# Performance work log

Hardware: AMD Instinct MI355X
Metric: run time of the kernel (lower is better)

## Reference

```python
import jax, jax.numpy as jnp
import numpy as np

B, H, L, D = 2, 16, 1024, 64
LMAX = 2048  # max_sequence_length: patterns built & normalized at LMAX, then sliced to L
PI = float(np.pi)


def _scale_pattern(freq):
    # pattern[h, t, d] = exp(i(t+ph)) + exp(i(2t+ph)) + exp(i(0.5t+ph)), ph = 2*pi*h/H
    # identical across d, so keep [H, L, 1] and broadcast over D
    phase = 2.0 * PI * jnp.arange(H, dtype=jnp.float32) / H          # [H]
    t = jnp.linspace(0.0, 2.0 * PI * freq, LMAX)                     # [LMAX]
    a1 = t[None, :] + phase[:, None]
    a2 = 2.0 * t[None, :] + phase[:, None]
    a3 = 0.5 * t[None, :] + phase[:, None]
    pr = jnp.cos(a1) + jnp.cos(a2) + jnp.cos(a3)                     # [H, LMAX]
    pi_ = jnp.sin(a1) + jnp.sin(a2) + jnp.sin(a3)
    norm = jnp.sqrt(jnp.sum(pr * pr + pi_ * pi_, axis=1, keepdims=True))  # over full LMAX
    pr, pi_ = pr / norm, pi_ / norm
    return pr[:, :L, None], pi_[:, :L, None]                          # [H, L, 1]


def _expert_total_pattern():
    # 8 experts x 3 aspects; pattern[t, d] = exp(i(f*t + 2*pi*d/D)), normalized per
    # column over LMAX (|exp|=1 -> norm sqrt(LMAX)). Elementwise complex multiply is
    # linear, so the expert stage equals x * sum(all patterns)/(sqrt(3)*sqrt(8)).
    freqs = np.array([[0.3 + 0.1 * i, 0.2 + 0.1 * i, 0.1 + 0.1 * i]
                      for i in range(8)], dtype=np.float32).reshape(-1)   # [24]
    t = jnp.linspace(0.0, 2.0 * PI, LMAX)                                 # [LMAX]
    phase_d = 2.0 * PI * jnp.arange(D, dtype=jnp.float32) / D             # [D]
    ang = jnp.asarray(freqs)[:, None, None] * t[None, :, None] + phase_d[None, None, :]  # [24, LMAX, D]
    col_norm = 1.0 / np.sqrt(float(LMAX))
    denom = np.sqrt(3.0) * np.sqrt(8.0)
    pr = jnp.sum(jnp.cos(ang), axis=0) * (col_norm / denom)               # [LMAX, D]
    pi_ = jnp.sum(jnp.sin(ang), axis=0) * (col_norm / denom)
    return pr[:L], pi_[:L]                                                # [L, D]


def _process_scale(Qr, Qi, Kr, Ki, Vr, Vi, pr, pi_):
    # complex elementwise pattern multiply
    Qpr = Qr * pr - Qi * pi_
    Qpi = Qr * pi_ + Qi * pr
    Kpr = Kr * pr - Ki * pi_
    Kpi = Kr * pi_ + Ki * pr
    # complex scores = Qp @ Kp^T (no conjugation, matching the torch code)
    sr = jnp.einsum('bhld,bhmd->bhlm', Qpr, Kpr) - jnp.einsum('bhld,bhmd->bhlm', Qpi, Kpi)
    si = jnp.einsum('bhld,bhmd->bhlm', Qpr, Kpi) + jnp.einsum('bhld,bhmd->bhlm', Qpi, Kpr)
    mag = jnp.sqrt(sr * sr + si * si) / np.sqrt(float(D))
    w = jax.nn.softmax(mag, axis=-1)
    return (jnp.einsum('bhlm,bhmd->bhld', w, Vr),
            jnp.einsum('bhlm,bhmd->bhld', w, Vi))


def reference(Q_real, Q_imag, K_real, K_imag, V_real, V_imag):
    scale_freqs = [1.0, 0.5, 0.25, 0.1]  # char, word, phrase, sentence
    acc_r = jnp.zeros_like(Q_real)
    acc_i = jnp.zeros_like(Q_real)
    for f in scale_freqs:
        pr, pi_ = _scale_pattern(f)
        o_r, o_i = _process_scale(Q_real, Q_imag, K_real, K_imag, V_real, V_imag, pr, pi_)
        acc_r = acc_r + o_r
        acc_i = acc_i + o_i
    inv = 1.0 / np.sqrt(float(len(scale_freqs)))
    acc_r = acc_r * inv
    acc_i = acc_i * inv
    # expert mixing (linear in x -> single fused complex elementwise multiply)
    epr, epi = _expert_total_pattern()  # [L, D], broadcast over B,H
    out_r = acc_r * epr - acc_i * epi
    out_i = acc_r * epi + acc_i * epr
    return jnp.stack([out_r, out_i], axis=0)  # [2, B, H, L, D] (real, imag)


def setup_inputs() -> dict:
    key = jax.random.key(0)
    ks = jax.random.split(key, 6)
    shape = (B, H, L, D)
    names = ['Q_real', 'Q_imag', 'K_real', 'K_imag', 'V_real', 'V_imag']
    return {n: jax.random.normal(k, shape, dtype=jnp.float32) for n, k in zip(names, ks)}
```

## Files before the change

### kernel.cpp

```cpp
#include <hip/hip_runtime.h>
#include <math.h>

typedef short bf16x8 __attribute__((ext_vector_type(8)));
typedef float f32x4 __attribute__((ext_vector_type(4)));

#define BDIM 256
constexpr int B_ = 2, H_ = 16, L_ = 1024, D_ = 64, LMAX_ = 2048;
constexpr int BH_ = B_ * H_;
constexpr float PI_F = 3.14159265358979323846f;

constexpr int WS_SVP = 0;
constexpr int WS_KBR = 65536;
constexpr int WS_KBI = WS_KBR + 1048576;
constexpr int WS_VTR = WS_KBI + 1048576;
constexpr int WS_VTI = WS_VTR + 1048576;

__device__ __forceinline__ unsigned short f2b(float x) {
    union { float f; unsigned u; } v; v.f = x;
    return (unsigned short)((v.u + 0x8000u) >> 16);
}
__device__ __forceinline__ float b2f(unsigned short x) {
    union { unsigned u; float f; } v; v.u = ((unsigned)x) << 16;
    return v.f;
}
__device__ __forceinline__ unsigned pk2(float a, float b) {
    union { float f; unsigned u; } va, vb; va.f = a; vb.f = b;
    return ((va.u + 0x8000u) >> 16) | ((vb.u + 0x8000u) & 0xFFFF0000u);
}
__device__ __forceinline__ uint4 pack4(const float4& a, const float4& b) {
    return make_uint4(pk2(a.x, a.y), pk2(a.z, a.w), pk2(b.x, b.y), pk2(b.z, b.w));
}
__device__ __forceinline__ unsigned cvtpk(float lo, float hi) {
    unsigned r;
    asm("v_cvt_pk_bf16_f32 %0, %1, %2" : "=v"(r) : "v"(lo), "v"(hi));
    return r;
}
__device__ __forceinline__ float vsqrt(float x) {
    float r;
    asm("v_sqrt_f32 %0, %1" : "=v"(r) : "v"(x));
    return r;
}

#define MFMA(a, b, c) __builtin_amdgcn_mfma_f32_16x16x32_bf16((a), (b), (c), 0, 0, 0)

__device__ __forceinline__ float a_val(int s, int l, float4 invn) {
    const float fr = (s == 0) ? 1.0f : (s == 1) ? 0.5f : (s == 2) ? 0.25f : 0.1f;
    const float iv = (s == 0) ? invn.x : (s == 1) ? invn.y : (s == 2) ? invn.z : invn.w;
    float t = (2.0f * PI_F * fr / (float)(LMAX_ - 1)) * (float)l;
    float m2 = 3.0f + 2.0f * cosf(t) + 2.0f * cosf(0.5f * t) + 2.0f * cosf(1.5f * t);
    return sqrtf(fmaxf(m2, 0.0f)) * iv;
}

__global__ __launch_bounds__(BDIM)
void prep_kernel(const float* __restrict__ Kr, const float* __restrict__ Ki,
                 const float* __restrict__ Vr, const float* __restrict__ Vi,
                 float* __restrict__ ws) {
    const int tid = threadIdx.x;
    const int blk = blockIdx.x;
    unsigned short* KbR = (unsigned short*)(ws + WS_KBR);
    unsigned short* KbI = (unsigned short*)(ws + WS_KBI);
    unsigned short* VtR = (unsigned short*)(ws + WS_VTR);
    unsigned short* VtI = (unsigned short*)(ws + WS_VTI);

    if (blk < 256) {
        const int comp = blk >> 7;
        const float* src = comp ? Ki : Kr;
        unsigned short* dst = comp ? KbI : KbR;
        size_t b0 = (size_t)(blk & 127) * 16384;
#pragma unroll
        for (int i = 0; i < 4; ++i) {
            size_t e = b0 + (size_t)(i * 256 + tid) * 16;
            float4 x0 = *(const float4*)(src + e);
            float4 x1 = *(const float4*)(src + e + 4);
            float4 x2 = *(const float4*)(src + e + 8);
            float4 x3 = *(const float4*)(src + e + 12);
            *(uint4*)(dst + e) = pack4(x0, x1);
            *(uint4*)(dst + e + 8) = pack4(x2, x3);
        }
    } else {
        __shared__ unsigned short sT[64 * 70];
        __shared__ float sRed[4 * 64];
        const int vb = blk - 256;
        const int comp = vb & 1, mt = (vb >> 1) & 15, bh = vb >> 5;
        const int m0 = mt * 64;
        const float* src = (comp ? Vi : Vr) + (size_t)bh * 65536 + (size_t)m0 * 64;
        unsigned short* dstA = (comp ? VtI : VtR) + (size_t)bh * 65536;
#pragma unroll
        for (int i = 0; i < 4; ++i) {
            int e = i * 256 + tid;
            int m = e >> 4, d4 = (e & 15) * 4;
            float4 x = *(const float4*)(src + (size_t)m * 64 + d4);
            *(uint2*)&sT[m * 70 + d4] = make_uint2(pk2(x.x, x.y), pk2(x.z, x.w));
        }
        {
            int d = tid & 63, grp = tid >> 6;
            float s = 0.0f;
#pragma unroll
            for (int k = 0; k < 16; ++k) s += src[(size_t)(grp * 16 + k) * 64 + d];
            sRed[grp * 64 + d] = s;
        }
        __syncthreads();
        {
            int d = tid >> 2, ms = (tid & 3) * 16;
            unsigned short v[16];
#pragma unroll
            for (int k = 0; k < 16; ++k) v[k] = sT[(ms + k) * 70 + d];
            unsigned short* dst = dstA + (size_t)d * 1024 + m0 + ms;
            *(uint4*)dst = make_uint4((unsigned)v[0] | ((unsigned)v[1] << 16),
                                      (unsigned)v[2] | ((unsigned)v[3] << 16),
                                      (unsigned)v[4] | ((unsigned)v[5] << 16),
                                      (unsigned)v[6] | ((unsigned)v[7] << 16));
            *(uint4*)(dst + 8) = make_uint4((unsigned)v[8] | ((unsigned)v[9] << 16),
                                            (unsigned)v[10] | ((unsigned)v[11] << 16),
                                            (unsigned)v[12] | ((unsigned)v[13] << 16),
                                            (unsigned)v[14] | ((unsigned)v[15] << 16));
        }
        if (tid < 64)
            ws[WS_SVP + comp * 32768 + bh * 1024 + tid * 16 + mt] =
                sRed[tid] + sRed[64 + tid] + sRed[128 + tid] + sRed[192 + tid];
    }
}

__device__ __forceinline__ void stage64s(const unsigned short* g0, int stride,
                                         unsigned short* lds, int w, int lane) {
#pragma unroll
    for (int i = 0; i < 2; ++i) {
        int c = w * 2 + i;
        int lrow = c * 8 + (lane >> 3);
        int lg = (lane & 7) ^ (lrow & 7);
        const unsigned short* src = g0 + (size_t)lrow * stride + lg * 8;
        __builtin_amdgcn_global_load_lds(
            (const __attribute__((address_space(1))) void*)src,
            (__attribute__((address_space(3))) void*)(lds + c * 512), 16, 0, 0);
    }
}
__device__ __forceinline__ bf16x8 ldfrag(const unsigned short* b, int row, int g) {
    return *(const bf16x8*)&b[row * 64 + ((g ^ (row & 7)) << 3)];
}

__global__ __launch_bounds__(BDIM, 2)
void attn_kernel(const float* __restrict__ Qr, const float* __restrict__ Qi,
                 const float* __restrict__ ws, float* __restrict__ out, float4 invn) {
    __shared__ unsigned short sK0[2][4096], sK1[2][4096];
    __shared__ unsigned short sV0[4096], sV1[4096];
    __shared__ unsigned short sE[4096];
    __shared__ unsigned short sMg[4096];
    __shared__ unsigned short sAmb[4 * 1032];
    __shared__ float sDen[4 * 64];

    const int tid = threadIdx.x;
    const int lane = tid & 63;
    const int w = tid >> 6;
    const int lo16 = lane & 15;
    const int quad = lane >> 4;
    const int blk = blockIdx.x;
    const int bh = (blk & 7) * 4 + (blk >> 7);
    const int qt = (blk >> 3) & 15;
    const int l0 = qt * 64;
    const size_t base = (size_t)bh * (L_ * D_);

    const unsigned short* gKr = (const unsigned short*)(ws + WS_KBR) + (size_t)bh * 65536;
    const unsigned short* gKi = (const unsigned short*)(ws + WS_KBI) + (size_t)bh * 65536;
    const unsigned short* gVr = (const unsigned short*)(ws + WS_VTR) + (size_t)bh * 65536;
    const unsigned short* gVi = (const unsigned short*)(ws + WS_VTI) + (size_t)bh * 65536;

    stage64s(gKr, 64, sK0[0], w, lane);
    stage64s(gKi, 64, sK1[0], w, lane);

    for (int e = tid; e < 4096; e += BDIM) {
        int s = e >> 10, l = e & 1023;
        sAmb[s * 1032 + l] = f2b(a_val(s, l, invn) * 0.125f);
    }

    bf16x8 fQr0, fQr1, fQi0, fQi1, fnQi0, fnQi1;
    {
        const int ql = l0 + w * 16 + lo16;
        const float* qr = Qr + base + (size_t)ql * 64;
        const float* qi = Qi + base + (size_t)ql * 64;
        float4 a0 = *(const float4*)(qr + quad * 8);
        float4 a1 = *(const float4*)(qr + quad * 8 + 4);
        float4 b0 = *(const float4*)(qr + 32 + quad * 8);
        float4 b1 = *(const float4*)(qr + 32 + quad * 8 + 4);
        *(uint4*)&fQr0 = pack4(a0, a1);
        *(uint4*)&fQr1 = pack4(b0, b1);
        a0 = *(const float4*)(qi + quad * 8);
        a1 = *(const float4*)(qi + quad * 8 + 4);
        b0 = *(const float4*)(qi + 32 + quad * 8);
        b1 = *(const float4*)(qi + 32 + quad * 8 + 4);
        *(uint4*)&fQi0 = pack4(a0, a1);
        *(uint4*)&fQi1 = pack4(b0, b1);
        uint4 t0 = *(uint4*)&fQi0, t1 = *(uint4*)&fQi1;
        t0.x ^= 0x80008000u; t0.y ^= 0x80008000u; t0.z ^= 0x80008000u; t0.w ^= 0x80008000u;
        t1.x ^= 0x80008000u; t1.y ^= 0x80008000u; t1.z ^= 0x80008000u; t1.w ^= 0x80008000u;
        *(uint4*)&fnQi0 = t0; *(uint4*)&fnQi1 = t1;
    }

    __syncthreads();

    bf16x8 uf1a = (bf16x8){0, 0, 0, 0, 0, 0, 0, 0};
    uf1a[0] = (short)f2b(b2f(sAmb[quad * 1032 + (l0 + w * 16 + lo16)]) *
                         (1.0f / 128.0f));

    f32x4 accM1 = (f32x4){0.f, 0.f, 0.f, 0.f};
    f32x4 aOutR[4], aOutI[4];
#pragma unroll
    for (int dt = 0; dt < 4; ++dt) {
        aOutR[dt] = (f32x4){0.f, 0.f, 0.f, 0.f};
        aOutI[dt] = (f32x4){0.f, 0.f, 0.f, 0.f};
    }

#pragma unroll 1
    for (int mt = 0; mt < 16; ++mt) {
        const int m0 = mt * 64;
        const int cur = mt & 1;
        stage64s(gVr + m0, 1024, sV0, w, lane);
        stage64s(gVi + m0, 1024, sV1, w, lane);
        if (mt < 15) {
            stage64s(gKr + (size_t)(m0 + 64) * 64, 64, sK0[cur ^ 1], w, lane);
            stage64s(gKi + (size_t)(m0 + 64) * 64, 64, sK1[cur ^ 1], w, lane);
        }
        const unsigned short* cK0 = sK0[cur];
        const unsigned short* cK1 = sK1[cur];

#pragma unroll
        for (int ct = 0; ct < 4; ++ct) {
            const int mrow = ct * 16 + lo16;
            bf16x8 kr0 = ldfrag(cK0, mrow, quad), kr1 = ldfrag(cK0, mrow, quad + 4);
            bf16x8 ki0 = ldfrag(cK1, mrow, quad), ki1 = ldfrag(cK1, mrow, quad + 4);
            f32x4 aR = (f32x4){0.f, 0.f, 0.f, 0.f};
            f32x4 aI = (f32x4){0.f, 0.f, 0.f, 0.f};
            __builtin_amdgcn_s_setprio(1);
            aR = MFMA(kr0, fQr0, aR);  aR = MFMA(kr1, fQr1, aR);
            aR = MFMA(ki0, fnQi0, aR); aR = MFMA(ki1, fnQi1, aR);
            aI = MFMA(ki0, fQr0, aI);  aI = MFMA(ki1, fQr1, aI);
            aI = MFMA(kr0, fQi0, aI);  aI = MFMA(kr1, fQi1, aI);
            __builtin_amdgcn_s_setprio(0);
            float mg0 = vsqrt(fmaf(aR[0], aR[0], aI[0] * aI[0]));
            float mg1 = vsqrt(fmaf(aR[1], aR[1], aI[1] * aI[1]));
            float mg2 = vsqrt(fmaf(aR[2], aR[2], aI[2] * aI[2]));
            float mg3 = vsqrt(fmaf(aR[3], aR[3], aI[3] * aI[3]));
            bf16x8 bf1 = (bf16x8){0, 0, 0, 0, 0, 0, 0, 0};
            bf1[0] = (short)sAmb[quad * 1032 + m0 + ct * 16 + lo16];
            f32x4 z = (f32x4){0.f, 0.f, 0.f, 0.f};
            f32x4 a1 = MFMA(bf1, uf1a, z);
            float p0 = mg0 * a1[0], p1 = mg1 * a1[1];
            float p2 = mg2 * a1[2], p3 = mg3 * a1[3];
            int l = w * 16 + lo16;
            int gph = (ct * 2 + (quad >> 1)) ^ (l & 7);
            *(uint2*)&sE[l * 64 + gph * 8 + (quad & 1) * 4] =
                make_uint2(cvtpk(p0, p1), cvtpk(p2, p3));
            *(uint2*)&sMg[l * 64 + gph * 8 + (quad & 1) * 4] =
                make_uint2(cvtpk(mg0, mg1), cvtpk(mg2, mg3));
        }
        {
            bf16x8 mf0 = ldfrag(sMg, w * 16 + lo16, quad);
            bf16x8 mf1 = ldfrag(sMg, w * 16 + lo16, quad + 4);
            bf16x8 b0 = (bf16x8){0, 0, 0, 0, 0, 0, 0, 0};
            bf16x8 b1 = (bf16x8){0, 0, 0, 0, 0, 0, 0, 0};
            if (lo16 < 4) {
                b0 = *(const bf16x8*)&sAmb[lo16 * 1032 + m0 + quad * 8];
                b1 = *(const bf16x8*)&sAmb[lo16 * 1032 + m0 + 32 + quad * 8];
            }
            accM1 = MFMA(mf0, b0, accM1);
            accM1 = MFMA(mf1, b1, accM1);
        }
        if (mt < 15) {
            asm volatile("s_waitcnt vmcnt(4)" ::: "memory");
        } else {
            asm volatile("s_waitcnt vmcnt(0)" ::: "memory");
        }
        __builtin_amdgcn_s_barrier();
        {
            bf16x8 pa0 = ldfrag(sE, w * 16 + lo16, quad);
            bf16x8 pa1 = ldfrag(sE, w * 16 + lo16, quad + 4);
            __builtin_amdgcn_s_setprio(1);
#pragma unroll
            for (int dt = 0; dt < 4; ++dt) {
                int dr = dt * 16 + lo16;
                bf16x8 vr0 = ldfrag(sV0, dr, quad), vr1 = ldfrag(sV0, dr, quad + 4);
                bf16x8 vi0 = ldfrag(sV1, dr, quad), vi1 = ldfrag(sV1, dr, quad + 4);
                aOutR[dt] = MFMA(pa0, vr0, aOutR[dt]);
                aOutR[dt] = MFMA(pa1, vr1, aOutR[dt]);
                aOutI[dt] = MFMA(pa0, vi0, aOutI[dt]);
                aOutI[dt] = MFMA(pa1, vi1, aOutI[dt]);
            }
            __builtin_amdgcn_s_setprio(0);
        }
        asm volatile("s_waitcnt vmcnt(0)" ::: "memory");
        __builtin_amdgcn_s_barrier();
    }

    if (lo16 < 4) {
#pragma unroll
        for (int reg = 0; reg < 4; ++reg) {
            int r = w * 16 + quad * 4 + reg;
            float alv = b2f(sAmb[lo16 * 1032 + (l0 + r)]) * 8.0f;
            sDen[lo16 * 64 + r] = 1.0f / (1024.0f + alv * accM1[reg]);
        }
    }
    float cden[4];
#pragma unroll
    for (int reg = 0; reg < 4; ++reg) {
        int r = w * 16 + quad * 4 + reg;
        cden[reg] = sDen[r] + sDen[64 + r] + sDen[128 + r] + sDen[192 + r];
    }

    const float cE = rsqrtf(2048.0f) * rsqrtf(24.0f);
    float eRr[4], eRi[4];
#pragma unroll
    for (int reg = 0; reg < 4; ++reg) {
        int lrow = l0 + w * 16 + quad * 4 + reg;
        float tl = (2.0f * PI_F / (float)(LMAX_ - 1)) * (float)lrow;
        float s1, c1;
        __sincosf(0.1f * tl, &s1, &c1);
        const float W[10] = {1.f, 2.f, 3.f, 3.f, 3.f, 3.f, 3.f, 3.f, 2.f, 1.f};
        float cr = c1, ci = s1;
        float er = W[0] * cr, ei = W[0] * ci;
#pragma unroll
        for (int k = 1; k < 10; ++k) {
            float nr = cr * c1 - ci * s1;
            float ni = cr * s1 + ci * c1;
            cr = nr; ci = ni;
            er = fmaf(W[k], cr, er);
            ei = fmaf(W[k], ci, ei);
        }
        eRr[reg] = er * cE;
        eRi[reg] = ei * cE;
    }

    const size_t ooff = (size_t)BH_ * L_ * D_;
#pragma unroll
    for (int dt = 0; dt < 4; ++dt) {
        int d = dt * 16 + lo16;
        const float* svp = ws + WS_SVP + bh * 1024 + (size_t)d * 16;
        float4 r0 = *(const float4*)(svp);
        float4 r1 = *(const float4*)(svp + 4);
        float4 r2 = *(const float4*)(svp + 8);
        float4 r3 = *(const float4*)(svp + 12);
        float svr = (r0.x + r0.y + r0.z + r0.w) + (r1.x + r1.y + r1.z + r1.w) +
                    (r2.x + r2.y + r2.z + r2.w) + (r3.x + r3.y + r3.z + r3.w);
        const float* svq = svp + 32768;
        r0 = *(const float4*)(svq);
        r1 = *(const float4*)(svq + 4);
        r2 = *(const float4*)(svq + 8);
        r3 = *(const float4*)(svq + 12);
        float svi = (r0.x + r0.y + r0.z + r0.w) + (r1.x + r1.y + r1.z + r1.w) +
                    (r2.x + r2.y + r2.z + r2.w) + (r3.x + r3.y + r3.z + r3.w);
        float sp, cp;
        __sincosf((2.0f * PI_F / 64.0f) * (float)d, &sp, &cp);
#pragma unroll
        for (int reg = 0; reg < 4; ++reg) {
            int lrow = l0 + w * 16 + quad * 4 + reg;
            float numR = fmaf(cden[reg], svr, aOutR[dt][reg]) * 0.5f;
            float numI = fmaf(cden[reg], svi, aOutI[dt][reg]) * 0.5f;
            float epr = cp * eRr[reg] - sp * eRi[reg];
            float epi = sp * eRr[reg] + cp * eRi[reg];
            size_t o = base + (size_t)lrow * 64 + d;
            out[o] = numR * epr - numI * epi;
            out[o + ooff] = numR * epi + numI * epr;
        }
    }
}

extern "C" void kernel_launch(void* const* d_in, const int* in_sizes, int n_in,
                              void* d_out, int out_size, void* d_ws, size_t ws_size,
                              hipStream_t stream) {
    const float* Qr = (const float*)d_in[0];
    const float* Qi = (const float*)d_in[1];
    const float* Kr = (const float*)d_in[2];
    const float* Ki = (const float*)d_in[3];
    const float* Vr = (const float*)d_in[4];
    const float* Vi = (const float*)d_in[5];
    float* ws = (float*)d_ws;
    float* out = (float*)d_out;

    const double fr[4] = {1.0, 0.5, 0.25, 0.1};
    float inv[4];
    for (int s = 0; s < 4; ++s) {
        double a = 2.0 * 3.14159265358979323846 * fr[s] / (double)(LMAX_ - 1);
        double S = 3.0 * LMAX_;
        const double mul[3] = {1.0, 0.5, 1.5};
        for (int k = 0; k < 3; ++k) {
            double x = a * mul[k];
            S += 2.0 * (cos(x * 1023.5) * sin(x * 1024.0) / sin(x * 0.5));
        }
        inv[s] = (float)(1.0 / sqrt(S));
    }
    float4 invn = make_float4(inv[0], inv[1], inv[2], inv[3]);

    prep_kernel<<<1280, BDIM, 0, stream>>>(Kr, Ki, Vr, Vi, ws);
    attn_kernel<<<512, BDIM, 0, stream>>>(Qr, Qi, ws, out, invn);
}
```

Baseline: 143.8 us.

## Widen attention blocks to 128 query rows with 8 waves sharing K/V tiles

Adds a 512-thread attention kernel that processes 128 query rows per block, so every K/V tile staged into LDS serves twice as many rows and global-to-LDS traffic per output is halved. Loading is split by wave role: waves 0-3 prefetch the next K tile while waves 4-7 load the current V tile, each with its own wait before the barrier. The kernel uses dynamic shared memory (~90KB) and falls back to the old kernel if the attribute call fails. The cost is half as many blocks (256) and larger LDS, which may lower occupancy and expose more latency.

Result: faster. 136.1 us (-5.3%).

```diff
diff --git a/kernel.cpp b/kernel.cpp
--- a/kernel.cpp
+++ b/kernel.cpp
@@ -5,6 +5,7 @@
 typedef float f32x4 __attribute__((ext_vector_type(4)));
 
 #define BDIM 256
+#define ADIM 512
 constexpr int B_ = 2, H_ = 16, L_ = 1024, D_ = 64, LMAX_ = 2048;
 constexpr int BH_ = B_ * H_;
 constexpr float PI_F = 3.14159265358979323846f;
@@ -138,15 +139,28 @@
     return *(const bf16x8*)&b[row * 64 + ((g ^ (row & 7)) << 3)];
 }
 
-__global__ __launch_bounds__(BDIM, 2)
-void attn_kernel(const float* __restrict__ Qr, const float* __restrict__ Qi,
-                 const float* __restrict__ ws, float* __restrict__ out, float4 invn) {
-    __shared__ unsigned short sK0[2][4096], sK1[2][4096];
-    __shared__ unsigned short sV0[4096], sV1[4096];
-    __shared__ unsigned short sE[4096];
-    __shared__ unsigned short sMg[4096];
-    __shared__ unsigned short sAmb[4 * 1032];
-    __shared__ float sDen[4 * 64];
+constexpr int OFF_DEN = 0;
+constexpr int OFF_K0  = 2048;
+constexpr int OFF_K1  = OFF_K0 + 16384;
+constexpr int OFF_V0  = OFF_K1 + 16384;
+constexpr int OFF_V1  = OFF_V0 + 8192;
+constexpr int OFF_E   = OFF_V1 + 8192;
+constexpr int OFF_MG  = OFF_E + 16384;
+constexpr int OFF_AMB = OFF_MG + 16384;
+constexpr int SMEM_BYTES = OFF_AMB + 8256;
+
+__global__ __launch_bounds__(ADIM, 2)
+void attn_kernel_w(const float* __restrict__ Qr, const float* __restrict__ Qi,
+                   const float* __restrict__ ws, float* __restrict__ out, float4 invn) {
+    extern __shared__ char smem[];
+    float* sDen = (float*)(smem + OFF_DEN);
+    unsigned short* sK0 = (unsigned short*)(smem + OFF_K0);
+    unsigned short* sK1 = (unsigned short*)(smem + OFF_K1);
+    unsigned short* sV0 = (unsigned short*)(smem + OFF_V0);
+    unsigned short* sV1 = (unsigned short*)(smem + OFF_V1);
+    unsigned short* sE  = (unsigned short*)(smem + OFF_E);
+    unsigned short* sMg = (unsigned short*)(smem + OFF_MG);
+    unsigned short* sAmb = (unsigned short*)(smem + OFF_AMB);
 
     const int tid = threadIdx.x;
     const int lane = tid & 63;
@@ -154,9 +168,9 @@
     const int lo16 = lane & 15;
     const int quad = lane >> 4;
     const int blk = blockIdx.x;
-    const int bh = (blk & 7) * 4 + (blk >> 7);
-    const int qt = (blk >> 3) & 15;
-    const int l0 = qt * 64;
+    const int bh = (blk & 7) * 4 + (blk >> 6);
+    const int qt = (blk >> 3) & 7;
+    const int l0 = qt * 128;
     const size_t base = (size_t)bh * (L_ * D_);
 
     const unsigned short* gKr = (const unsigned short*)(ws + WS_KBR) + (size_t)bh * 65536;
@@ -164,10 +178,12 @@
     const unsigned short* gVr = (const unsigned short*)(ws + WS_VTR) + (size_t)bh * 65536;
     const unsigned short* gVi = (const unsigned short*)(ws + WS_VTI) + (size_t)bh * 65536;
 
-    stage64s(gKr, 64, sK0[0], w, lane);
-    stage64s(gKi, 64, sK1[0], w, lane);
-
-    for (int e = tid; e < 4096; e += BDIM) {
+    if (w < 4) {
+        stage64s(gKr, 64, sK0, w, lane);
+        stage64s(gKi, 64, sK1, w, lane);
+    }
+
+    for (int e = tid; e < 4096; e += ADIM) {
         int s = e >> 10, l = e & 1023;
         sAmb[s * 1032 + l] = f2b(a_val(s, l, invn) * 0.125f);
     }
@@ -213,14 +229,15 @@
     for (int mt = 0; mt < 16; ++mt) {
         const int m0 = mt * 64;
         const int cur = mt & 1;
-        stage64s(gVr + m0, 1024, sV0, w, lane);
-        stage64s(gVi + m0, 1024, sV1, w, lane);
-        if (mt < 15) {
-            stage64s(gKr + (size_t)(m0 + 64) * 64, 64, sK0[cur ^ 1], w, lane);
-            stage64s(gKi + (size_t)(m0 + 64) * 64, 64, sK1[cur ^ 1], w, lane);
-        }
-        const unsigned short* cK0 = sK0[cur];
-        const unsigned short* cK1 = sK1[cur];
+        if (w >= 4) {
+            stage64s(gVr + m0, 1024, sV0, w - 4, lane);
+            stage64s(gVi + m0, 1024, sV1, w - 4, lane);
+        } else if (mt < 15) {
+            stage64s(gKr + (size_t)(m0 + 64) * 64, 64, sK0 + (cur ^ 1) * 4096, w, lane);
+            stage64s(gKi + (size_t)(m0 + 64) * 64, 64, sK1 + (cur ^ 1) * 4096, w, lane);
+        }
+        const unsigned short* cK0 = sK0 + cur * 4096;
+        const unsigned short* cK1 = sK1 + cur * 4096;
 
 #pragma unroll
         for (int ct = 0; ct < 4; ++ct) {
@@ -264,11 +281,7 @@
             accM1 = MFMA(mf0, b0, accM1);
             accM1 = MFMA(mf1, b1, accM1);
         }
-        if (mt < 15) {
-            asm volatile("s_waitcnt vmcnt(4)" ::: "memory");
-        } else {
-            asm volatile("s_waitcnt vmcnt(0)" ::: "memory");
-        }
+        if (w >= 4) asm volatile("s_waitcnt vmcnt(0)" ::: "memory");
         __builtin_amdgcn_s_barrier();
         {
             bf16x8 pa0 = ldfrag(sE, w * 16 + lo16, quad);
@@ -286,7 +299,7 @@
             }
             __builtin_amdgcn_s_setprio(0);
         }
-        asm volatile("s_waitcnt vmcnt(0)" ::: "memory");
+        if (w < 4) asm volatile("s_waitcnt vmcnt(0)" ::: "memory");
         __builtin_amdgcn_s_barrier();
     }
 
@@ -295,14 +308,14 @@
         for (int reg = 0; reg < 4; ++reg) {
             int r = w * 16 + quad * 4 + reg;
             float alv = b2f(sAmb[lo16 * 1032 + (l0 + r)]) * 8.0f;
-            sDen[lo16 * 64 + r] = 1.0f / (1024.0f + alv * accM1[reg]);
+            sDen[lo16 * 128 + r] = 1.0f / (1024.0f + alv * accM1[reg]);
         }
     }
     float cden[4];
 #pragma unroll
     for (int reg = 0; reg < 4; ++reg) {
         int r = w * 16 + quad * 4 + reg;
-        cden[reg] = sDen[r] + sDen[64 + r] + sDen[128 + r] + sDen[192 + r];
+        cden[reg] = sDen[r] + sDen[128 + r] + sDen[256 + r] + sDen[384 + r];
     }
 
     const float cE = rsqrtf(2048.0f) * rsqrtf(24.0f);
@@ -362,6 +375,230 @@
     }
 }
 
+__global__ __launch_bounds__(BDIM, 2)
+void attn_kernel(const float* __restrict__ Qr, const float* __restrict__ Qi,
+                 const float* __restrict__ ws, float* __restrict__ out, float4 invn) {
+    __shared__ unsigned short sK0[2][4096], sK1[2][4096];
+    __shared__ unsigned short sV0[4096], sV1[4096];
+    __shared__ unsigned short sE[4096];
+    __shared__ unsigned short sMg[4096];
+    __shared__ unsigned short sAmb[4 * 1032];
+    __shared__ float sDen[4 * 64];
+
+    const int tid = threadIdx.x;
+    const int lane = tid & 63;
+    const int w = tid >> 6;
+    const int lo16 = lane & 15;
+    const int quad = lane >> 4;
+    const int blk = blockIdx.x;
+    const int bh = (blk & 7) * 4 + (blk >> 7);
+    const int qt = (blk >> 3) & 15;
+    const int l0 = qt * 64;
+    const size_t base = (size_t)bh * (L_ * D_);
+
+    const unsigned short* gKr = (const unsigned short*)(ws + WS_KBR) + (size_t)bh * 65536;
+    const unsigned short* gKi = (const unsigned short*)(ws + WS_KBI) + (size_t)bh * 65536;
+    const unsigned short* gVr = (const unsigned short*)(ws + WS_VTR) + (size_t)bh * 65536;
+    const unsigned short* gVi = (const unsigned short*)(ws + WS_VTI) + (size_t)bh * 65536;
+
+    stage64s(gKr, 64, sK0[0], w, lane);
+    stage64s(gKi, 64, sK1[0], w, lane);
+
+    for (int e = tid; e < 4096; e += BDIM) {
+        int s = e >> 10, l = e & 1023;
+        sAmb[s * 1032 + l] = f2b(a_val(s, l, invn) * 0.125f);
+    }
+
+    bf16x8 fQr0, fQr1, fQi0, fQi1, fnQi0, fnQi1;
+    {
+        const int ql = l0 + w * 16 + lo16;
+        const float* qr = Qr + base + (size_t)ql * 64;
+        const float* qi = Qi + base + (size_t)ql * 64;
+        float4 a0 = *(const float4*)(qr + quad * 8);
+        float4 a1 = *(const float4*)(qr + quad * 8 + 4);
+        float4 b0 = *(const float4*)(qr + 32 + quad * 8);
+        float4 b1 = *(const float4*)(qr + 32 + quad * 8 + 4);
+        *(uint4*)&fQr0 = pack4(a0, a1);
+        *(uint4*)&fQr1 = pack4(b0, b1);
+        a0 = *(const float4*)(qi + quad * 8);
+        a1 = *(const float4*)(qi + quad * 8 + 4);
+        b0 = *(const float4*)(qi + 32 + quad * 8);
+        b1 = *(const float4*)(qi + 32 + quad * 8 + 4);
+        *(uint4*)&fQi0 = pack4(a0, a1);
+        *(uint4*)&fQi1 = pack4(b0, b1);
+        uint4 t0 = *(uint4*)&fQi0, t1 = *(uint4*)&fQi1;
+        t0.x ^= 0x80008000u; t0.y ^= 0x80008000u; t0.z ^= 0x80008000u; t0.w ^= 0x80008000u;
+        t1.x ^= 0x80008000u; t1.y ^= 0x80008000u; t1.z ^= 0x80008000u; t1.w ^= 0x80008000u;
+        *(uint4*)&fnQi0 = t0; *(uint4*)&fnQi1 = t1;
+    }
+
+    __syncthreads();
+
+    bf16x8 uf1a = (bf16x8){0, 0, 0, 0, 0, 0, 0, 0};
+    uf1a[0] = (short)f2b(b2f(sAmb[quad * 1032 + (l0 + w * 16 + lo16)]) *
+                         (1.0f / 128.0f));
+
+    f32x4 accM1 = (f32x4){0.f, 0.f, 0.f, 0.f};
+    f32x4 aOutR[4], aOutI[4];
+#pragma unroll
+    for (int dt = 0; dt < 4; ++dt) {
+        aOutR[dt] = (f32x4){0.f, 0.f, 0.f, 0.f};
+        aOutI[dt] = (f32x4){0.f, 0.f, 0.f, 0.f};
+    }
+
+#pragma unroll 1
+    for (int mt = 0; mt < 16; ++mt) {
+        const int m0 = mt * 64;
+        const int cur = mt & 1;
+        stage64s(gVr + m0, 1024, sV0, w, lane);
+        stage64s(gVi + m0, 1024, sV1, w, lane);
+        if (mt < 15) {
+            stage64s(gKr + (size_t)(m0 + 64) * 64, 64, sK0[cur ^ 1], w, lane);
+            stage64s(gKi + (size_t)(m0 + 64) * 64, 64, sK1[cur ^ 1], w, lane);
+        }
+        const unsigned short* cK0 = sK0[cur];
+        const unsigned short* cK1 = sK1[cur];
+
+#pragma unroll
+        for (int ct = 0; ct < 4; ++ct) {
+            const int mrow = ct * 16 + lo16;
+            bf16x8 kr0 = ldfrag(cK0, mrow, quad), kr1 = ldfrag(cK0, mrow, quad + 4);
+            bf16x8 ki0 = ldfrag(cK1, mrow, quad), ki1 = ldfrag(cK1, mrow, quad + 4);
+            f32x4 aR = (f32x4){0.f, 0.f, 0.f, 0.f};
+            f32x4 aI = (f32x4){0.f, 0.f, 0.f, 0.f};
+            __builtin_amdgcn_s_setprio(1);
+            aR = MFMA(kr0, fQr0, aR);  aR = MFMA(kr1, fQr1, aR);
+            aR = MFMA(ki0, fnQi0, aR); aR = MFMA(ki1, fnQi1, aR);
+            aI = MFMA(ki0, fQr0, aI);  aI = MFMA(ki1, fQr1, aI);
+            aI = MFMA(kr0, fQi0, aI);  aI = MFMA(kr1, fQi1, aI);
+            __builtin_amdgcn_s_setprio(0);
+            float mg0 = vsqrt(fmaf(aR[0], aR[0], aI[0] * aI[0]));
+            float mg1 = vsqrt(fmaf(aR[1], aR[1], aI[1] * aI[1]));
+            float mg2 = vsqrt(fmaf(aR[2], aR[2], aI[2] * aI[2]));
+            float mg3 = vsqrt(fmaf(aR[3], aR[3], aI[3] * aI[3]));
+            bf16x8 bf1 = (bf16x8){0, 0, 0, 0, 0, 0, 0, 0};
+            bf1[0] = (short)sAmb[quad * 1032 + m0 + ct * 16 + lo16];
+            f32x4 z = (f32x4){0.f, 0.f, 0.f, 0.f};
+            f32x4 a1 = MFMA(bf1, uf1a, z);
+            float p0 = mg0 * a1[0], p1 = mg1 * a1[1];
+            float p2 = mg2 * a1[2], p3 = mg3 * a1[3];
+            int l = w * 16 + lo16;
+            int gph = (ct * 2 + (quad >> 1)) ^ (l & 7);
+            *(uint2*)&sE[l * 64 + gph * 8 + (quad & 1) * 4] =
+                make_uint2(cvtpk(p0, p1), cvtpk(p2, p3));
+            *(uint2*)&sMg[l * 64 + gph * 8 + (quad & 1) * 4] =
+                make_uint2(cvtpk(mg0, mg1), cvtpk(mg2, mg3));
+        }
+        {
+            bf16x8 mf0 = ldfrag(sMg, w * 16 + lo16, quad);
+            bf16x8 mf1 = ldfrag(sMg, w * 16 + lo16, quad + 4);
+            bf16x8 b0 = (bf16x8){0, 0, 0, 0, 0, 0, 0, 0};
+            bf16x8 b1 = (bf16x8){0, 0, 0, 0, 0, 0, 0, 0};
+            if (lo16 < 4) {
+                b0 = *(const bf16x8*)&sAmb[lo16 * 1032 + m0 + quad * 8];
+                b1 = *(const bf16x8*)&sAmb[lo16 * 1032 + m0 + 32 + quad * 8];
+            }
+            accM1 = MFMA(mf0, b0, accM1);
+            accM1 = MFMA(mf1, b1, accM1);
+        }
+        if (mt < 15) {
+            asm volatile("s_waitcnt vmcnt(4)" ::: "memory");
+        } else {
+            asm volatile("s_waitcnt vmcnt(0)" ::: "memory");
+        }
+        __builtin_amdgcn_s_barrier();
+        {
+            bf16x8 pa0 = ldfrag(sE, w * 16 + lo16, quad);
+            bf16x8 pa1 = ldfrag(sE, w * 16 + lo16, quad + 4);
+            __builtin_amdgcn_s_setprio(1);
+#pragma unroll
+            for (int dt = 0; dt < 4; ++dt) {
+                int dr = dt * 16 + lo16;
+                bf16x8 vr0 = ldfrag(sV0, dr, quad), vr1 = ldfrag(sV0, dr, quad + 4);
+                bf16x8 vi0 = ldfrag(sV1, dr, quad), vi1 = ldfrag(sV1, dr, quad + 4);
+                aOutR[dt] = MFMA(pa0, vr0, aOutR[dt]);
+                aOutR[dt] = MFMA(pa1, vr1, aOutR[dt]);
+                aOutI[dt] = MFMA(pa0, vi0, aOutI[dt]);
+                aOutI[dt] = MFMA(pa1, vi1, aOutI[dt]);
+            }
+            __builtin_amdgcn_s_setprio(0);
+        }
+        asm volatile("s_waitcnt vmcnt(0)" ::: "memory");
+        __builtin_amdgcn_s_barrier();
+    }
+
+    if (lo16 < 4) {
+#pragma unroll
+        for (int reg = 0; reg < 4; ++reg) {
+            int r = w * 16 + quad * 4 + reg;
+            float alv = b2f(sAmb[lo16 * 1032 + (l0 + r)]) * 8.0f;
+            sDen[lo16 * 64 + r] = 1.0f / (1024.0f + alv * accM1[reg]);
+        }
+    }
+    float cden[4];
+#pragma unroll
+    for (int reg = 0; reg < 4; ++reg) {
+        int r = w * 16 + quad * 4 + reg;
+        cden[reg] = sDen[r] + sDen[64 + r] + sDen[128 + r] + sDen[192 + r];
+    }
+
+    const float cE = rsqrtf(2048.0f) * rsqrtf(24.0f);
+    float eRr[4], eRi[4];
+#pragma unroll
+    for (int reg = 0; reg < 4; ++reg) {
+        int lrow = l0 + w * 16 + quad * 4 + reg;
+        float tl = (2.0f * PI_F / (float)(LMAX_ - 1)) * (float)lrow;
+        float s1, c1;
+        __sincosf(0.1f * tl, &s1, &c1);
+        const float W[10] = {1.f, 2.f, 3.f, 3.f, 3.f, 3.f, 3.f, 3.f, 2.f, 1.f};
+        float cr = c1, ci = s1;
+        float er = W[0] * cr, ei = W[0] * ci;
+#pragma unroll
+        for (int k = 1; k < 10; ++k) {
+            float nr = cr * c1 - ci * s1;
+            float ni = cr * s1 + ci * c1;
+            cr = nr; ci = ni;
+            er = fmaf(W[k], cr, er);
+            ei = fmaf(W[k], ci, ei);
+        }
+        eRr[reg] = er * cE;
+        eRi[reg] = ei * cE;
+    }
+
+    const size_t ooff = (size_t)BH_ * L_ * D_;
+#pragma unroll
+    for (int dt = 0; dt < 4; ++dt) {
+        int d = dt * 16 + lo16;
+        const float* svp = ws + WS_SVP + bh * 1024 + (size_t)d * 16;
+        float4 r0 = *(const float4*)(svp);
+        float4 r1 = *(const float4*)(svp + 4);
+        float4 r2 = *(const float4*)(svp + 8);
+        float4 r3 = *(const float4*)(svp + 12);
+        float svr = (r0.x + r0.y + r0.z + r0.w) + (r1.x + r1.y + r1.z + r1.w) +
+                    (r2.x + r2.y + r2.z + r2.w) + (r3.x + r3.y + r3.z + r3.w);
+        const float* svq = svp + 32768;
+        r0 = *(const float4*)(svq);
+        r1 = *(const float4*)(svq + 4);
+        r2 = *(const float4*)(svq + 8);
+        r3 = *(const float4*)(svq + 12);
+        float svi = (r0.x + r0.y + r0.z + r0.w) + (r1.x + r1.y + r1.z + r1.w) +
+                    (r2.x + r2.y + r2.z + r2.w) + (r3.x + r3.y + r3.z + r3.w);
+        float sp, cp;
+        __sincosf((2.0f * PI_F / 64.0f) * (float)d, &sp, &cp);
+#pragma unroll
+        for (int reg = 0; reg < 4; ++reg) {
+            int lrow = l0 + w * 16 + quad * 4 + reg;
+            float numR = fmaf(cden[reg], svr, aOutR[dt][reg]) * 0.5f;
+            float numI = fmaf(cden[reg], svi, aOutI[dt][reg]) * 0.5f;
+            float epr = cp * eRr[reg] - sp * eRi[reg];
+            float epi = sp * eRr[reg] + cp * eRi[reg];
+            size_t o = base + (size_t)lrow * 64 + d;
+            out[o] = numR * epr - numI * epi;
+            out[o + ooff] = numR * epi + numI * epr;
+        }
+    }
+}
+
 extern "C" void kernel_launch(void* const* d_in, const int* in_sizes, int n_in,
                               void* d_out, int out_size, void* d_ws, size_t ws_size,
                               hipStream_t stream) {
@@ -389,5 +626,16 @@
     float4 invn = make_float4(inv[0], inv[1], inv[2], inv[3]);
 
     prep_kernel<<<1280, BDIM, 0, stream>>>(Kr, Ki, Vr, Vi, ws);
-    attn_kernel<<<512, BDIM, 0, stream>>>(Qr, Qi, ws, out, invn);
-}
+
+    static int wideOK = -1;
+    if (wideOK < 0) {
+        hipError_t e = hipFuncSetAttribute(
+            reinterpret_cast<const void*>(attn_kernel_w),
+            hipFuncAttributeMaxDynamicSharedMemorySize, SMEM_BYTES);
+        wideOK = (e == hipSuccess) ? 1 : 0;
+    }
+    if (wideOK)
+        attn_kernel_w<<<256, ADIM, SMEM_BYTES, stream>>>(Qr, Qi, ws, out, invn);
+    else
+        attn_kernel<<<512, BDIM, 0, stream>>>(Qr, Qi, ws, out, invn);
+}
```
